# Optimization experiments

Measured on AMD Instinct MI355X. Metric: run time of the kernel, lower is better.

Reference implementation:

```python
import jax, jax.numpy as jnp
import numpy as np

SEGMENT_LENGTHS = [1024, 2048, 4096]
DILATION_RATES = [1, 2, 4]


def setup_inputs() -> dict:
    key = jax.random.key(0)
    kq, kk, kv = jax.random.split(key, 3)
    shape = (2, 4096, 12, 64)  # [batch, seq_len, num_heads, head_dim]
    return {
        "query": jax.random.normal(kq, shape, dtype=jnp.float32),
        "key": jax.random.normal(kk, shape, dtype=jnp.float32),
        "value": jax.random.normal(kv, shape, dtype=jnp.float32),
        "is_causal": 0,
    }


def _group_attention(q, k, v, g, r, offset, is_causal):
    """Dilated segment attention for one head group.

    q/k/v: [b, n, hg, d] (head slice for this group).
    Segments of length g; within each segment attend only at positions
    offset, offset+r, ... (m = g // r tokens). Output scattered back to
    those positions; other positions are zero (LongNet semantics).
    """
    b, n, h, d = q.shape
    s = n // g  # number of segments
    m = g // r  # dilated tokens per segment
    idx = offset + r * jnp.arange(m)
    qs = q.reshape(b, s, g, h, d)[:, :, idx]  # [b, s, m, h, d]
    ks = k.reshape(b, s, g, h, d)[:, :, idx]
    vs = v.reshape(b, s, g, h, d)[:, :, idx]
    scale = 1.0 / jnp.sqrt(jnp.asarray(d, dtype=q.dtype))
    scores = jnp.einsum("bsqhd,bskhd->bshqk", qs, ks) * scale  # [b, s, h, m, m]
    if is_causal:
        mask = jnp.tril(jnp.ones((m, m), dtype=bool))
        scores = jnp.where(mask, scores, jnp.finfo(scores.dtype).min)
    probs = jax.nn.softmax(scores, axis=-1)
    o = jnp.einsum("bshqk,bskhd->bsqhd", probs, vs)  # [b, s, m, h, d]
    out = jnp.zeros((b, s, g, h, d), dtype=q.dtype).at[:, :, idx].set(o)
    return out.reshape(b, n, h, d)


def reference(query, key, value, is_causal):
    # dist not initialized -> sequence-parallel split/gather are identity;
    # forward reduces to ImprovedDilatedAttention on full tensors.
    b, n, h, d = query.shape
    ngroups = len(SEGMENT_LENGTHS)
    hpg = h // ngroups  # heads per group (disjoint head slices)
    causal = bool(is_causal)
    outs = []
    for i, (g, r) in enumerate(zip(SEGMENT_LENGTHS, DILATION_RATES)):
        offset = i % r
        hmin, hmax = i * hpg, (i + 1) * hpg
        outs.append(
            _group_attention(
                query[:, :, hmin:hmax],
                key[:, :, hmin:hmax],
                value[:, :, hmin:hmax],
                g, r, offset, causal,
            )
        )
    return jnp.concatenate(outs, axis=2)  # [b, n, h, d]
```

## Files before the change

### kernel.cpp

```cpp
#include <hip/hip_runtime.h>
#include <hip/hip_bf16.h>

typedef __attribute__((ext_vector_type(8))) short short8;
typedef __attribute__((ext_vector_type(4))) float f32x4;

#define NTILE 16

static __device__ __forceinline__ unsigned pk2(float x, float y) {
  __hip_bfloat162 h = __float22bfloat162_rn(make_float2(x, y));
  unsigned u; __builtin_memcpy(&u, &h, 4); return u;
}

static __device__ __forceinline__ short8 cvt8(float4 a, float4 b) {
  union { unsigned u[4]; short8 s; } r;
  r.u[0] = pk2(a.x, a.y); r.u[1] = pk2(a.z, a.w);
  r.u[2] = pk2(b.x, b.y); r.u[3] = pk2(b.z, b.w);
  return r.s;
}

static __device__ __forceinline__ void gll16(const void* g, void* l) {
  __builtin_amdgcn_global_load_lds(
      (__attribute__((address_space(1))) void*)const_cast<void*>(g),
      (__attribute__((address_space(3))) void*)(l), 16, 0, 0);
}

struct InstInfo { long base0; int stride; };
static __device__ __forceinline__ InstInfo decode_inst(int inst) {
  const int gi    = (inst < 32) ? 0 : ((inst < 48) ? 1 : 2);
  const int local = inst - ((gi == 0) ? 0 : ((gi == 1) ? 32 : 48));
  const int segs  = 4 >> gi;
  const int g     = 1024 << gi;
  const int offs  = gi;
  const int h     = local & 3;
  const int rem   = local >> 2;
  const int seg   = rem & (segs - 1);
  const int b     = rem >> (2 - gi);
  const int hh    = gi * 4 + h;
  InstInfo r;
  r.base0  = ((long)(b * 4096 + seg * g + offs) * 12 + hh) * 64;
  r.stride = (1 << gi) * 768;
  return r;
}

__global__ __launch_bounds__(256)
void pack_kv(const float* __restrict__ Kg, const float* __restrict__ Vg,
             unsigned short* __restrict__ Ks, unsigned short* __restrict__ Vts,
             float* __restrict__ Og)
{
  __shared__ float vtmp[64][65];
  const int tid   = threadIdx.x;
  const int lid   = blockIdx.x;
  const int inst  = lid % 56;
  const int chunk = lid / 56;
  const int gi    = (inst < 32) ? 0 : ((inst < 48) ? 1 : 2);
  InstInfo I = decode_inst(inst);

  {
    const int tok = tid >> 2, part = tid & 3;
    const long ro = I.base0 + (long)(chunk * 64 + tok) * I.stride + part * 16;
    const float4 k0 = *(const float4*)(Kg + ro);
    const float4 k1 = *(const float4*)(Kg + ro + 4);
    const float4 k2 = *(const float4*)(Kg + ro + 8);
    const float4 k3 = *(const float4*)(Kg + ro + 12);
    uint4 ka, kb;
    ka.x = pk2(k0.x,k0.y); ka.y = pk2(k0.z,k0.w); ka.z = pk2(k1.x,k1.y); ka.w = pk2(k1.z,k1.w);
    kb.x = pk2(k2.x,k2.y); kb.y = pk2(k2.z,k2.w); kb.z = pk2(k3.x,k3.y); kb.w = pk2(k3.z,k3.w);
    unsigned short* kd = Ks + ((long)inst*1024 + chunk*64 + tok)*64;
    const int c0 = (2*part)     ^ (tok & 7);
    const int c1 = (2*part + 1) ^ (tok & 7);
    *(uint4*)(kd + c0*8) = ka;
    *(uint4*)(kd + c1*8) = kb;

    const float4 w0 = *(const float4*)(Vg + ro);
    const float4 w1 = *(const float4*)(Vg + ro + 4);
    const float4 w2 = *(const float4*)(Vg + ro + 8);
    const float4 w3 = *(const float4*)(Vg + ro + 12);
    float* c = &vtmp[part*16][0] + tok;
    c[0*65]=w0.x;  c[1*65]=w0.y;  c[2*65]=w0.z;  c[3*65]=w0.w;
    c[4*65]=w1.x;  c[5*65]=w1.y;  c[6*65]=w1.z;  c[7*65]=w1.w;
    c[8*65]=w2.x;  c[9*65]=w2.y;  c[10*65]=w2.z; c[11*65]=w2.w;
    c[12*65]=w3.x; c[13*65]=w3.y; c[14*65]=w3.z; c[15*65]=w3.w;
  }
  __syncthreads();
  {
    const int d = tid >> 2, kp = tid & 3;
    float v[16];
#pragma unroll
    for (int i = 0; i < 16; ++i) v[i] = vtmp[d][kp*16 + i];
    unsigned short* vd = Vts + ((long)inst*64 + d)*1024 + chunk*64;
#pragma unroll
    for (int s = 0; s < 2; ++s) {
      const int pos = (kp*2 + s) ^ (d & 7);
      uint4 w;
      w.x = pk2(v[8*s+0], v[8*s+1]); w.y = pk2(v[8*s+2], v[8*s+3]);
      w.z = pk2(v[8*s+4], v[8*s+5]); w.w = pk2(v[8*s+6], v[8*s+7]);
      *(uint4*)(vd + pos*8) = w;
    }
  }

  const float4 z4 = make_float4(0.f, 0.f, 0.f, 0.f);
  if (gi == 1) {
    for (int i = tid; i < 64*16; i += 256) {
      const int t = i >> 4, pp = i & 15;
      float* op = Og + I.base0 + (long)(chunk*128 + 2*t + 0 - 1) * 768 + pp*4;
      *(float4*)op = z4;
    }
  } else if (gi == 2) {
    for (int i = tid; i < 192*16; i += 256) {
      const int row_i = i >> 4, pp = i & 15;
      const int t = row_i / 3, ddi = row_i - 3*t;
      const int dd = ddi + (ddi >= 2 ? 1 : 0);
      float* op = Og + I.base0 + (long)(chunk*256 + 4*t + dd - 2) * 768 + pp*4;
      *(float4*)op = z4;
    }
  }
}

__global__ __launch_bounds__(256, 2)
void dilated_attn2(const float* __restrict__ Qg,
                   const unsigned short* __restrict__ Ks,
                   const unsigned short* __restrict__ Vts,
                   const int* __restrict__ causal_flag,
                   float* __restrict__ Og)
{
  __shared__ __align__(16) unsigned short K_lds[2][64][64];
  __shared__ __align__(16) unsigned short V_lds[2][64][64];
  __shared__ __align__(16) unsigned short P_lds[4][16][64];

  const int tid  = threadIdx.x;
  const int wave = tid >> 6;
  const int lane = tid & 63;
  const int l15  = lane & 15;
  const int l4   = lane >> 4;
  const int sw   = l15 & 7;

  const int lid  = blockIdx.x;
  const int inst = lid % 56;
  const int qt   = lid / 56;
  InstInfo I = decode_inst(inst);
  const int causal = *causal_flag;

  const float qscale = 0.125f * 1.44269504088896340736f;
  short8 b_q[2][2];
  int qrowf[2];
#pragma unroll
  for (int qf = 0; qf < 2; ++qf) {
    qrowf[qf] = qt*128 + wave*32 + qf*16 + l15;
    const float* qp = Qg + I.base0 + (long)qrowf[qf] * I.stride + l4 * 8;
#pragma unroll
    for (int ks = 0; ks < 2; ++ks) {
      float4 v0 = *(const float4*)(qp + ks*32);
      float4 v1 = *(const float4*)(qp + ks*32 + 4);
      v0.x *= qscale; v0.y *= qscale; v0.z *= qscale; v0.w *= qscale;
      v1.x *= qscale; v1.y *= qscale; v1.z *= qscale; v1.w *= qscale;
      b_q[qf][ks] = cvt8(v0, v1);
    }
  }

  short8 ones8;
  {
    union { unsigned u[4]; short8 s; } r;
    r.u[0] = r.u[1] = r.u[2] = r.u[3] = 0x3F803F80u;
    ones8 = r.s;
  }

  const unsigned short* KsI  = Ks  + (long)inst * (1024*64);
  const unsigned short* VtsI = Vts + (long)inst * (64*1024);
  const int vrow = lane >> 3;
  const int vcol = (lane & 7) * 8;

  const long koffA = (long)(wave*8     + vrow)*64 + vcol;
  const long koffB = (long)((wave+4)*8 + vrow)*64 + vcol;
  const long voffA = (long)(wave*8     + vrow)*1024 + vcol;
  const long voffB = (long)((wave+4)*8 + vrow)*1024 + vcol;
  const int  colA  = ((l4 ^ sw) & 7) * 8;
  const int  colB  = (((4 + l4) ^ sw) & 7) * 8;
  const unsigned short* krow0 = &K_lds[0][l15][0];
  const unsigned short* krow1 = &K_lds[1][l15][0];
  const unsigned short* vrow0 = &V_lds[0][l15][0];
  const unsigned short* vrow1 = &V_lds[1][l15][0];
  unsigned short* pw = &P_lds[wave][l15][0];
  int pwo[4];
#pragma unroll
  for (int n = 0; n < 4; ++n)
    pwo[n] = (((2*n + (l4 >> 1)) ^ sw) & 7)*8 + (l4 & 1)*4;
  const int pro0 = colA;
  const int pro1 = colB;

  f32x4 Oacc[2][4];
  f32x4 accl[2];
#pragma unroll
  for (int qf = 0; qf < 2; ++qf) {
    accl[qf] = (f32x4){0.f,0.f,0.f,0.f};
#pragma unroll
    for (int n = 0; n < 4; ++n) Oacc[qf][n] = (f32x4){0.f,0.f,0.f,0.f};
  }

#define STAGE_G(BUF, KP, VP) do {                                              \
    gll16((KP) + koffA, &K_lds[BUF][wave*8][0]);                               \
    gll16((KP) + koffB, &K_lds[BUF][(wave+4)*8][0]);                           \
    gll16((VP) + voffA, &V_lds[BUF][wave*8][0]);                               \
    gll16((VP) + voffB, &V_lds[BUF][(wave+4)*8][0]);                           \
  } while (0)

#define COMPUTE(CUR, KT) do {                                                  \
    f32x4 S0[4], S1[4];                                                        \
    __builtin_amdgcn_s_setprio(1);                                             \
    _Pragma("unroll")                                                          \
    for (int n = 0; n < 4; ++n) {                                              \
      short8 kA = *(const short8*)(krow##CUR + n*1024 + colA);                 \
      short8 kB = *(const short8*)(krow##CUR + n*1024 + colB);                 \
      f32x4 a0 = (f32x4){0.f,0.f,0.f,0.f};                                     \
      a0 = __builtin_amdgcn_mfma_f32_16x16x32_bf16(kA, b_q[0][0], a0, 0,0,0);  \
      a0 = __builtin_amdgcn_mfma_f32_16x16x32_bf16(kB, b_q[0][1], a0, 0,0,0);  \
      S0[n] = a0;                                                              \
      f32x4 a1 = (f32x4){0.f,0.f,0.f,0.f};                                     \
      a1 = __builtin_amdgcn_mfma_f32_16x16x32_bf16(kA, b_q[1][0], a1, 0,0,0);  \
      a1 = __builtin_amdgcn_mfma_f32_16x16x32_bf16(kB, b_q[1][1], a1, 0,0,0);  \
      S1[n] = a1;                                                              \
    }                                                                          \
    __builtin_amdgcn_s_setprio(0);                                             \
    if (causal) {                                                              \
      _Pragma("unroll")                                                        \
      for (int n = 0; n < 4; ++n)                                              \
        _Pragma("unroll")                                                      \
        for (int j = 0; j < 4; ++j) {                                          \
          int ktok = (KT)*64 + n*16 + l4*4 + j;                                \
          if (ktok > qrowf[0]) S0[n][j] = -INFINITY;                           \
          if (ktok > qrowf[1]) S1[n][j] = -INFINITY;                           \
        }                                                                      \
    }                                                                          \
    short8 ap0a, ap0b, ap1a, ap1b;                                             \
    {                                                                \
      _Pragma("unroll")                                                        \
      for (int n = 0; n < 4; ++n) {                                            \
        unsigned u0 = pk2(__builtin_amdgcn_exp2f(S0[n][0]),                    \
                          __builtin_amdgcn_exp2f(S0[n][1]));                   \
        unsigned u1 = pk2(__builtin_amdgcn_exp2f(S0[n][2]),                    \
                          __builtin_amdgcn_exp2f(S0[n][3]));                   \
        *(uint2*)(pw + pwo[n]) = make_uint2(u0, u1);                           \
      }                                                                        \
      ap0a = *(const short8*)(pw + pro0);                                      \
      ap0b = *(const short8*)(pw + pro1);                                      \
      accl[0] = __builtin_amdgcn_mfma_f32_16x16x32_bf16(ap0a, ones8, accl[0], 0,0,0); \
      accl[0] = __builtin_amdgcn_mfma_f32_16x16x32_bf16(ap0b, ones8, accl[0], 0,0,0); \
    }                                                                          \
    {                                                                \
      _Pragma("unroll")                                                        \
      for (int n = 0; n < 4; ++n) {                                            \
        unsigned u0 = pk2(__builtin_amdgcn_exp2f(S1[n][0]),                    \
                          __builtin_amdgcn_exp2f(S1[n][1]));                   \
        unsigned u1 = pk2(__builtin_amdgcn_exp2f(S1[n][2]),                    \
                          __builtin_amdgcn_exp2f(S1[n][3]));                   \
        *(uint2*)(pw + pwo[n]) = make_uint2(u0, u1);                           \
      }                                                                        \
      ap1a = *(const short8*)(pw + pro0);                                      \
      ap1b = *(const short8*)(pw + pro1);                                      \
      accl[1] = __builtin_amdgcn_mfma_f32_16x16x32_bf16(ap1a, ones8, accl[1], 0,0,0); \
      accl[1] = __builtin_amdgcn_mfma_f32_16x16x32_bf16(ap1b, ones8, accl[1], 0,0,0); \
    }                                                                          \
    _Pragma("unroll")                                                          \
    for (int n = 0; n < 4; ++n) {                                              \
      short8 bv0 = *(const short8*)(vrow##CUR + n*1024 + colA);                \
      short8 bv1 = *(const short8*)(vrow##CUR + n*1024 + colB);                \
      __builtin_amdgcn_s_setprio(1);                                           \
      Oacc[0][n] = __builtin_amdgcn_mfma_f32_16x16x32_bf16(ap0a, bv0, Oacc[0][n], 0,0,0); \
      Oacc[0][n] = __builtin_amdgcn_mfma_f32_16x16x32_bf16(ap0b, bv1, Oacc[0][n], 0,0,0); \
      Oacc[1][n] = __builtin_amdgcn_mfma_f32_16x16x32_bf16(ap1a, bv0, Oacc[1][n], 0,0,0); \
      Oacc[1][n] = __builtin_amdgcn_mfma_f32_16x16x32_bf16(ap1b, bv1, Oacc[1][n], 0,0,0); \
      __builtin_amdgcn_s_setprio(0);                                           \
    }                                                                          \
  } while (0)

  STAGE_G(0, KsI, VtsI);
  __syncthreads();

  const unsigned short* kp1 = KsI + 4096;
  const unsigned short* kp2 = KsI + 8192;
  const unsigned short* vp1 = VtsI + 64;
  const unsigned short* vp2 = VtsI + 128;

  for (int p = 0; p < NTILE/2; ++p) {
    const int kt = 2*p;
    STAGE_G(1, kp1, vp1);
    COMPUTE(0, kt);
    __syncthreads();
    if (p < NTILE/2 - 1) STAGE_G(0, kp2, vp2);
    COMPUTE(1, kt + 1);
    __syncthreads();
    kp1 += 8192; kp2 += 8192; vp1 += 128; vp2 += 128;
  }

  float* ob = Og + I.base0;
#pragma unroll
  for (int qf = 0; qf < 2; ++qf)
#pragma unroll
    for (int j = 0; j < 4; ++j) {
      const float inv = 1.f / accl[qf][j];
      const int qrow = qt*128 + wave*32 + qf*16 + l4*4 + j;
      float* op = ob + (long)qrow * I.stride;
#pragma unroll
      for (int n = 0; n < 4; ++n)
        op[n*16 + l15] = Oacc[qf][n][j] * inv;
    }
}

#define LDP 72
__global__ __launch_bounds__(512, 4)
void dilated_attn_fb(const float* __restrict__ Qg,
                     const float* __restrict__ Kg,
                     const float* __restrict__ Vg,
                     const int* __restrict__ causal_flag,
                     float* __restrict__ Og)
{
  __shared__ __align__(16) unsigned short K_lds[2][64][LDP];
  __shared__ __align__(16) unsigned short Vt_lds[2][64][LDP];
  __shared__ __align__(16) unsigned short P_lds[8][16][LDP];

  const int tid  = threadIdx.x;
  const int wave = tid >> 6;
  const int lane = tid & 63;
  const int l15  = lane & 15;
  const int l4   = lane >> 4;
  const int qt   = blockIdx.x;
  InstInfo I = decode_inst(blockIdx.y);
  const int causal = *causal_flag;

  const float qscale = 0.125f * 1.44269504088896340736f;
  short8 b_q[2];
  {
    const int qrow = qt * 128 + wave * 16 + l15;
    const float* qp = Qg + I.base0 + (long)qrow * I.stride + l4 * 8;
#pragma unroll
    for (int ks = 0; ks < 2; ++ks) {
      float4 v0 = *(const float4*)(qp + ks * 32);
      float4 v1 = *(const float4*)(qp + ks * 32 + 4);
      v0.x *= qscale; v0.y *= qscale; v0.z *= qscale; v0.w *= qscale;
      v1.x *= qscale; v1.y *= qscale; v1.z *= qscale; v1.w *= qscale;
      b_q[ks] = cvt8(v0, v1);
    }
  }
  float m_run = -INFINITY, l_run = 0.f;
  f32x4 Oacc[4];
#pragma unroll
  for (int n = 0; n < 4; ++n) Oacc[n] = (f32x4){0.f,0.f,0.f,0.f};
  const int tt  = tid >> 3;
  const int cb8 = tid & 7;
  const float* kbase = Kg + I.base0 + cb8 * 8;
  const float* vbase = Vg + I.base0 + cb8 * 8;
#define STAGE_FB(BUF, A0, A1, W0, W1) do {                                     \
    *(short8*)&K_lds[BUF][tt][cb8 * 8] = cvt8(A0, A1);                         \
    unsigned p01 = pk2(W0.x, W0.y), p23 = pk2(W0.z, W0.w);                     \
    unsigned p45 = pk2(W1.x, W1.y), p67 = pk2(W1.z, W1.w);                     \
    const int col = (((tt >> 3) ^ cb8) << 3) | (tt & 7);                       \
    Vt_lds[BUF][cb8*8+0][col] = (unsigned short)(p01 & 0xffff);                \
    Vt_lds[BUF][cb8*8+1][col] = (unsigned short)(p01 >> 16);                   \
    Vt_lds[BUF][cb8*8+2][col] = (unsigned short)(p23 & 0xffff);                \
    Vt_lds[BUF][cb8*8+3][col] = (unsigned short)(p23 >> 16);                   \
    Vt_lds[BUF][cb8*8+4][col] = (unsigned short)(p45 & 0xffff);                \
    Vt_lds[BUF][cb8*8+5][col] = (unsigned short)(p45 >> 16);                   \
    Vt_lds[BUF][cb8*8+6][col] = (unsigned short)(p67 & 0xffff);                \
    Vt_lds[BUF][cb8*8+7][col] = (unsigned short)(p67 >> 16);                   \
  } while (0)
  {
    const long ro = (long)tt * I.stride;
    float4 k0 = *(const float4*)(kbase + ro);
    float4 k1 = *(const float4*)(kbase + ro + 4);
    float4 w0 = *(const float4*)(vbase + ro);
    float4 w1 = *(const float4*)(vbase + ro + 4);
    STAGE_FB(0, k0, k1, w0, w1);
  }
  __syncthreads();
  const int qrow_me = qt * 128 + wave * 16 + l15;
  for (int kt = 0; kt < NTILE; ++kt) {
    const int bsel = kt & 1;
    float4 nk0, nk1, nw0, nw1;
    const bool have_next = (kt + 1 < NTILE);
    if (have_next) {
      const long ro = (long)((kt + 1) * 64 + tt) * I.stride;
      nk0 = *(const float4*)(kbase + ro);
      nk1 = *(const float4*)(kbase + ro + 4);
      nw0 = *(const float4*)(vbase + ro);
      nw1 = *(const float4*)(vbase + ro + 4);
    }
    f32x4 S[4];
#pragma unroll
    for (int n = 0; n < 4; ++n) {
      short8 ak0 = *(const short8*)&K_lds[bsel][n*16 + l15][l4*8];
      short8 ak1 = *(const short8*)&K_lds[bsel][n*16 + l15][32 + l4*8];
      f32x4 acc = (f32x4){0.f,0.f,0.f,0.f};
      acc = __builtin_amdgcn_mfma_f32_16x16x32_bf16(ak0, b_q[0], acc, 0,0,0);
      acc = __builtin_amdgcn_mfma_f32_16x16x32_bf16(ak1, b_q[1], acc, 0,0,0);
      S[n] = acc;
    }
    if (causal) {
#pragma unroll
      for (int n = 0; n < 4; ++n)
#pragma unroll
        for (int j = 0; j < 4; ++j) {
          int ktok = kt*64 + n*16 + l4*4 + j;
          if (ktok > qrow_me) S[n][j] = -INFINITY;
        }
    }
    float pmax = S[0][0];
#pragma unroll
    for (int n = 0; n < 4; ++n)
#pragma unroll
      for (int j = 0; j < 4; ++j) pmax = fmaxf(pmax, S[n][j]);
    pmax = fmaxf(pmax, __shfl_xor(pmax, 16));
    pmax = fmaxf(pmax, __shfl_xor(pmax, 32));
    if (!__all(pmax - m_run <= 8.f)) {
      float mn = fmaxf(m_run, pmax);
      float corr = exp2f(m_run - mn);
      m_run = mn; l_run *= corr;
      float cq[4];
#pragma unroll
      for (int j = 0; j < 4; ++j) cq[j] = __shfl(corr, l4*4 + j, 16);
#pragma unroll
      for (int n = 0; n < 4; ++n)
#pragma unroll
        for (int j = 0; j < 4; ++j) Oacc[n][j] *= cq[j];
    }
    float psum = 0.f; unsigned up[4][2];
#pragma unroll
    for (int n = 0; n < 4; ++n)
#pragma unroll
      for (int s = 0; s < 2; ++s) {
        float p0 = exp2f(S[n][2*s]   - m_run);
        float p1 = exp2f(S[n][2*s+1] - m_run);
        psum += p0 + p1; up[n][s] = pk2(p0, p1);
      }
    l_run += psum;
#pragma unroll
    for (int n = 0; n < 4; ++n)
      *(uint2*)&P_lds[wave][l15][n*16 + l4*4] = make_uint2(up[n][0], up[n][1]);
    {
      short8 ap0 = *(const short8*)&P_lds[wave][l15][l4*8];
      short8 ap1 = *(const short8*)&P_lds[wave][l15][32 + l4*8];
#pragma unroll
      for (int n = 0; n < 4; ++n) {
        const int dsw = (2*n + (l15 >> 3)) & 7;
        short8 bv0 = *(const short8*)&Vt_lds[bsel][n*16 + l15][((l4 ^ dsw) & 7)*8];
        short8 bv1 = *(const short8*)&Vt_lds[bsel][n*16 + l15][(((4 + l4) ^ dsw) & 7)*8];
        Oacc[n] = __builtin_amdgcn_mfma_f32_16x16x32_bf16(ap0, bv0, Oacc[n], 0,0,0);
        Oacc[n] = __builtin_amdgcn_mfma_f32_16x16x32_bf16(ap1, bv1, Oacc[n], 0,0,0);
      }
    }
    if (have_next) STAGE_FB(bsel ^ 1, nk0, nk1, nw0, nw1);
    __syncthreads();
  }
  l_run += __shfl_xor(l_run, 16);
  l_run += __shfl_xor(l_run, 32);
  float lq[4];
#pragma unroll
  for (int j = 0; j < 4; ++j) lq[j] = __shfl(l_run, l4*4 + j, 16);
  float* ob = Og + I.base0;
#pragma unroll
  for (int j = 0; j < 4; ++j) {
    const float inv = 1.f / lq[j];
    const int qrow = qt*128 + wave*16 + l4*4 + j;
    float* op = ob + (long)qrow * I.stride;
#pragma unroll
    for (int n = 0; n < 4; ++n)
      op[n*16 + l15] = Oacc[n][j] * inv;
  }
}

extern "C" void kernel_launch(void* const* d_in, const int* in_sizes, int n_in,
                              void* d_out, int out_size, void* d_ws, size_t ws_size,
                              hipStream_t stream) {
  const float* Q = (const float*)d_in[0];
  const float* K = (const float*)d_in[1];
  const float* V = (const float*)d_in[2];
  const int* causal = (const int*)d_in[3];
  float* out = (float*)d_out;

  const size_t per = 56ull * 1024 * 64;
  const size_t need_pack = 2 * per * sizeof(unsigned short);

  if (ws_size >= need_pack) {
    unsigned short* Ks  = (unsigned short*)d_ws;
    unsigned short* Vts = Ks + per;
    pack_kv<<<896, 256, 0, stream>>>(K, V, Ks, Vts, out);
    dilated_attn2<<<448, 256, 0, stream>>>(Q, Ks, Vts, causal, out);
  } else {
    (void)hipMemsetAsync(d_out, 0, (size_t)out_size * sizeof(float), stream);
    dilated_attn_fb<<<dim3(8, 56), 512, 0, stream>>>(Q, K, V, causal, out);
  }
}
```

Before: 40.22 us.

## Split each KV tile across two wave groups and merge partial outputs in LDS

Doubles the block to 512 threads. Each of the two 4-wave halves processes a different 32-key half of every 64-key tile for the same 128 queries, which halves each wave's MFMA and exp work per tile. The partial O accumulators and row sums from the second half are reduced through LDS in the epilogue. The no-max softmax makes the split-K merge a plain sum. In exchange it adds an extra barrier, LDS traffic in the epilogue, and higher register and LDS pressure per CU.

```diff
diff --git a/kernel.cpp b/kernel.cpp
--- a/kernel.cpp
+++ b/kernel.cpp
@@ -116,16 +116,16 @@
   }
 }
 
-__global__ __launch_bounds__(256, 2)
+__global__ __launch_bounds__(512, 2)
 void dilated_attn2(const float* __restrict__ Qg,
                    const unsigned short* __restrict__ Ks,
                    const unsigned short* __restrict__ Vts,
                    const int* __restrict__ causal_flag,
                    float* __restrict__ Og)
 {
-  __shared__ __align__(16) unsigned short K_lds[2][64][64];
-  __shared__ __align__(16) unsigned short V_lds[2][64][64];
-  __shared__ __align__(16) unsigned short P_lds[4][16][64];
+  __shared__ __align__(16) unsigned short KV_lds[4][64][64];
+  __shared__ __align__(16) unsigned short P_lds[8][16][64];
+  __shared__ float Lx[4][32];
 
   const int tid  = threadIdx.x;
   const int wave = tid >> 6;
@@ -133,6 +133,9 @@
   const int l15  = lane & 15;
   const int l4   = lane >> 4;
   const int sw   = l15 & 7;
+  const int qh   = wave & 3;
+  const int kh   = wave >> 2;
+  const int khb  = kh * 32;
 
   const int lid  = blockIdx.x;
   const int inst = lid % 56;
@@ -145,7 +148,7 @@
   int qrowf[2];
 #pragma unroll
   for (int qf = 0; qf < 2; ++qf) {
-    qrowf[qf] = qt*128 + wave*32 + qf*16 + l15;
+    qrowf[qf] = qt*128 + qh*32 + qf*16 + l15;
     const float* qp = Qg + I.base0 + (long)qrowf[qf] * I.stride + l4 * 8;
 #pragma unroll
     for (int ks = 0; ks < 2; ++ks) {
@@ -169,23 +172,21 @@
   const int vrow = lane >> 3;
   const int vcol = (lane & 7) * 8;
 
-  const long koffA = (long)(wave*8     + vrow)*64 + vcol;
-  const long koffB = (long)((wave+4)*8 + vrow)*64 + vcol;
-  const long voffA = (long)(wave*8     + vrow)*1024 + vcol;
-  const long voffB = (long)((wave+4)*8 + vrow)*1024 + vcol;
-  const int  colA  = ((l4 ^ sw) & 7) * 8;
-  const int  colB  = (((4 + l4) ^ sw) & 7) * 8;
-  const unsigned short* krow0 = &K_lds[0][l15][0];
-  const unsigned short* krow1 = &K_lds[1][l15][0];
-  const unsigned short* vrow0 = &V_lds[0][l15][0];
-  const unsigned short* vrow1 = &V_lds[1][l15][0];
+  const long koff = (long)(wave*8 + vrow)*64 + vcol;
+  const long voff = (long)(wave*8 + vrow)*1024 + vcol;
+  const int  colA = ((l4 ^ sw) & 7) * 8;
+  const int  colB = (((4 + l4) ^ sw) & 7) * 8;
+  const int  vcb  = (((kh*4 + l4) ^ sw) & 7) * 8;
+  const unsigned short* krow0 = &KV_lds[0][khb + l15][0];
+  const unsigned short* krow1 = &KV_lds[1][khb + l15][0];
+  const unsigned short* vb0   = &KV_lds[2][l15][0];
+  const unsigned short* vb1   = &KV_lds[3][l15][0];
   unsigned short* pw = &P_lds[wave][l15][0];
-  int pwo[4];
-#pragma unroll
-  for (int n = 0; n < 4; ++n)
+  int pwo[2];
+#pragma unroll
+  for (int n = 0; n < 2; ++n)
     pwo[n] = (((2*n + (l4 >> 1)) ^ sw) & 7)*8 + (l4 & 1)*4;
-  const int pro0 = colA;
-  const int pro1 = colB;
+  const int pro = colA;
 
   f32x4 Oacc[2][4];
   f32x4 accl[2];
@@ -197,19 +198,17 @@
   }
 
 #define STAGE_G(BUF, KP, VP) do {                                              \
-    gll16((KP) + koffA, &K_lds[BUF][wave*8][0]);                               \
-    gll16((KP) + koffB, &K_lds[BUF][(wave+4)*8][0]);                           \
-    gll16((VP) + voffA, &V_lds[BUF][wave*8][0]);                               \
-    gll16((VP) + voffB, &V_lds[BUF][(wave+4)*8][0]);                           \
+    gll16((KP) + koff, &KV_lds[BUF][wave*8][0]);                               \
+    gll16((VP) + voff, &KV_lds[2+(BUF)][wave*8][0]);                           \
   } while (0)
 
 #define COMPUTE(CUR, KT) do {                                                  \
-    f32x4 S0[4], S1[4];                                                        \
+    f32x4 S0[2], S1[2];                                                        \
     __builtin_amdgcn_s_setprio(1);                                             \
     _Pragma("unroll")                                                          \
-    for (int n = 0; n < 4; ++n) {                                              \
-      short8 kA = *(const short8*)(krow##CUR + n*1024 + colA);                 \
-      short8 kB = *(const short8*)(krow##CUR + n*1024 + colB);                 \
+    for (int n = 0; n < 2; ++n) {                                              \
+      short8 kA = *(const short8*)(krow##CUR + n*16*64 + colA);                \
+      short8 kB = *(const short8*)(krow##CUR + n*16*64 + colB);                \
       f32x4 a0 = (f32x4){0.f,0.f,0.f,0.f};                                     \
       a0 = __builtin_amdgcn_mfma_f32_16x16x32_bf16(kA, b_q[0][0], a0, 0,0,0);  \
       a0 = __builtin_amdgcn_mfma_f32_16x16x32_bf16(kB, b_q[0][1], a0, 0,0,0);  \
@@ -222,52 +221,45 @@
     __builtin_amdgcn_s_setprio(0);                                             \
     if (causal) {                                                              \
       _Pragma("unroll")                                                        \
-      for (int n = 0; n < 4; ++n)                                              \
+      for (int n = 0; n < 2; ++n)                                              \
         _Pragma("unroll")                                                      \
         for (int j = 0; j < 4; ++j) {                                          \
-          int ktok = (KT)*64 + n*16 + l4*4 + j;                                \
+          int ktok = (KT)*64 + khb + n*16 + l4*4 + j;                          \
           if (ktok > qrowf[0]) S0[n][j] = -INFINITY;                           \
           if (ktok > qrowf[1]) S1[n][j] = -INFINITY;                           \
         }                                                                      \
     }                                                                          \
-    short8 ap0a, ap0b, ap1a, ap1b;                                             \
+    short8 ap0, ap1;                                                           \
     {                                                                \
       _Pragma("unroll")                                                        \
-      for (int n = 0; n < 4; ++n) {                                            \
+      for (int n = 0; n < 2; ++n) {                                            \
         unsigned u0 = pk2(__builtin_amdgcn_exp2f(S0[n][0]),                    \
                           __builtin_amdgcn_exp2f(S0[n][1]));                   \
         unsigned u1 = pk2(__builtin_amdgcn_exp2f(S0[n][2]),                    \
                           __builtin_amdgcn_exp2f(S0[n][3]));                   \
         *(uint2*)(pw + pwo[n]) = make_uint2(u0, u1);                           \
       }                                                                        \
-      ap0a = *(const short8*)(pw + pro0);                                      \
-      ap0b = *(const short8*)(pw + pro1);                                      \
-      accl[0] = __builtin_amdgcn_mfma_f32_16x16x32_bf16(ap0a, ones8, accl[0], 0,0,0); \
-      accl[0] = __builtin_amdgcn_mfma_f32_16x16x32_bf16(ap0b, ones8, accl[0], 0,0,0); \
+      ap0 = *(const short8*)(pw + pro);                                        \
+      accl[0] = __builtin_amdgcn_mfma_f32_16x16x32_bf16(ap0, ones8, accl[0], 0,0,0); \
     }                                                                          \
     {                                                                \
       _Pragma("unroll")                                                        \
-      for (int n = 0; n < 4; ++n) {                                            \
+      for (int n = 0; n < 2; ++n) {                                            \
         unsigned u0 = pk2(__builtin_amdgcn_exp2f(S1[n][0]),                    \
                           __builtin_amdgcn_exp2f(S1[n][1]));                   \
         unsigned u1 = pk2(__builtin_amdgcn_exp2f(S1[n][2]),                    \
                           __builtin_amdgcn_exp2f(S1[n][3]));                   \
         *(uint2*)(pw + pwo[n]) = make_uint2(u0, u1);                           \
       }                                                                        \
-      ap1a = *(const short8*)(pw + pro0);                                      \
-      ap1b = *(const short8*)(pw + pro1);                                      \
-      accl[1] = __builtin_amdgcn_mfma_f32_16x16x32_bf16(ap1a, ones8, accl[1], 0,0,0); \
-      accl[1] = __builtin_amdgcn_mfma_f32_16x16x32_bf16(ap1b, ones8, accl[1], 0,0,0); \
+      ap1 = *(const short8*)(pw + pro);                                        \
+      accl[1] = __builtin_amdgcn_mfma_f32_16x16x32_bf16(ap1, ones8, accl[1], 0,0,0); \
     }                                                                          \
     _Pragma("unroll")                                                          \
     for (int n = 0; n < 4; ++n) {                                              \
-      short8 bv0 = *(const short8*)(vrow##CUR + n*1024 + colA);                \
-      short8 bv1 = *(const short8*)(vrow##CUR + n*1024 + colB);                \
+      short8 bv = *(const short8*)(vb##CUR + n*16*64 + vcb);                   \
       __builtin_amdgcn_s_setprio(1);                                           \
-      Oacc[0][n] = __builtin_amdgcn_mfma_f32_16x16x32_bf16(ap0a, bv0, Oacc[0][n], 0,0,0); \
-      Oacc[0][n] = __builtin_amdgcn_mfma_f32_16x16x32_bf16(ap0b, bv1, Oacc[0][n], 0,0,0); \
-      Oacc[1][n] = __builtin_amdgcn_mfma_f32_16x16x32_bf16(ap1a, bv0, Oacc[1][n], 0,0,0); \
-      Oacc[1][n] = __builtin_amdgcn_mfma_f32_16x16x32_bf16(ap1b, bv1, Oacc[1][n], 0,0,0); \
+      Oacc[0][n] = __builtin_amdgcn_mfma_f32_16x16x32_bf16(ap0, bv, Oacc[0][n], 0,0,0); \
+      Oacc[1][n] = __builtin_amdgcn_mfma_f32_16x16x32_bf16(ap1, bv, Oacc[1][n], 0,0,0); \
       __builtin_amdgcn_s_setprio(0);                                           \
     }                                                                          \
   } while (0)
@@ -291,18 +283,36 @@
     kp1 += 8192; kp2 += 8192; vp1 += 128; vp2 += 128;
   }
 
-  float* ob = Og + I.base0;
-#pragma unroll
-  for (int qf = 0; qf < 2; ++qf)
-#pragma unroll
-    for (int j = 0; j < 4; ++j) {
-      const float inv = 1.f / accl[qf][j];
-      const int qrow = qt*128 + wave*32 + qf*16 + l4*4 + j;
-      float* op = ob + (long)qrow * I.stride;
-#pragma unroll
-      for (int n = 0; n < 4; ++n)
-        op[n*16 + l15] = Oacc[qf][n][j] * inv;
-    }
+  float* Ox = (float*)&KV_lds[0][0][0];
+  if (kh == 1) {
+#pragma unroll
+    for (int qf = 0; qf < 2; ++qf)
+#pragma unroll
+      for (int j = 0; j < 4; ++j) {
+        const int r = qf*16 + l4*4 + j;
+        float* dst = Ox + (qh*32 + r)*64;
+#pragma unroll
+        for (int n = 0; n < 4; ++n) dst[n*16 + l15] = Oacc[qf][n][j];
+        if (l15 == 0) Lx[qh][r] = accl[qf][j];
+      }
+  }
+  __syncthreads();
+  if (kh == 0) {
+    float* ob = Og + I.base0;
+#pragma unroll
+    for (int qf = 0; qf < 2; ++qf)
+#pragma unroll
+      for (int j = 0; j < 4; ++j) {
+        const int r = qf*16 + l4*4 + j;
+        const float* src = Ox + (qh*32 + r)*64;
+        const float inv = 1.f / (accl[qf][j] + Lx[qh][r]);
+        const int qrow = qt*128 + qh*32 + r;
+        float* op = ob + (long)qrow * I.stride;
+#pragma unroll
+        for (int n = 0; n < 4; ++n)
+          op[n*16 + l15] = (Oacc[qf][n][j] + src[n*16 + l15]) * inv;
+      }
+  }
 }
 
 #define LDP 72
@@ -482,7 +492,7 @@
     unsigned short* Ks  = (unsigned short*)d_ws;
     unsigned short* Vts = Ks + per;
     pack_kv<<<896, 256, 0, stream>>>(K, V, Ks, Vts, out);
-    dilated_attn2<<<448, 256, 0, stream>>>(Q, Ks, Vts, causal, out);
+    dilated_attn2<<<448, 512, 0, stream>>>(Q, Ks, Vts, causal, out);
   } else {
     (void)hipMemsetAsync(d_out, 0, (size_t)out_size * sizeof(float), stream);
     dilated_attn_fb<<<dim3(8, 56), 512, 0, stream>>>(Q, K, V, causal, out);
```

Result: slower. 41.15 us (+2.3%).

## Load K/V fragments directly from global into registers, drop LDS staging

Applied to the files above, without the earlier changes.

The attention kernel no longer stages K and V tiles into shared memory with global_load_lds and barriers. Each lane now loads its MFMA operand fragments straight from global memory into registers, double-buffered across tiles. The pre-pass drops its XOR swizzle and writes K and transposed V in a plain layout. This removes LDS traffic and the per-tile __syncthreads, at the cost of more register pressure and repeated global/L2 reads, since the four waves each fetch the same K/V data.

```diff
diff --git a/kernel.cpp b/kernel.cpp
--- a/kernel.cpp
+++ b/kernel.cpp
@@ -16,12 +16,6 @@
   r.u[0] = pk2(a.x, a.y); r.u[1] = pk2(a.z, a.w);
   r.u[2] = pk2(b.x, b.y); r.u[3] = pk2(b.z, b.w);
   return r.s;
-}
-
-static __device__ __forceinline__ void gll16(const void* g, void* l) {
-  __builtin_amdgcn_global_load_lds(
-      (__attribute__((address_space(1))) void*)const_cast<void*>(g),
-      (__attribute__((address_space(3))) void*)(l), 16, 0, 0);
 }
 
 struct InstInfo { long base0; int stride; };
@@ -65,11 +59,8 @@
     uint4 ka, kb;
     ka.x = pk2(k0.x,k0.y); ka.y = pk2(k0.z,k0.w); ka.z = pk2(k1.x,k1.y); ka.w = pk2(k1.z,k1.w);
     kb.x = pk2(k2.x,k2.y); kb.y = pk2(k2.z,k2.w); kb.z = pk2(k3.x,k3.y); kb.w = pk2(k3.z,k3.w);
-    unsigned short* kd = Ks + ((long)inst*1024 + chunk*64 + tok)*64;
-    const int c0 = (2*part)     ^ (tok & 7);
-    const int c1 = (2*part + 1) ^ (tok & 7);
-    *(uint4*)(kd + c0*8) = ka;
-    *(uint4*)(kd + c1*8) = kb;
+    unsigned short* kd = Ks + ((long)inst*1024 + chunk*64 + tok)*64 + part*16;
+    *(uint4*)kd = ka; *(uint4*)(kd + 8) = kb;
 
     const float4 w0 = *(const float4*)(Vg + ro);
     const float4 w1 = *(const float4*)(Vg + ro + 4);
@@ -87,15 +78,13 @@
     float v[16];
 #pragma unroll
     for (int i = 0; i < 16; ++i) v[i] = vtmp[d][kp*16 + i];
-    unsigned short* vd = Vts + ((long)inst*64 + d)*1024 + chunk*64;
-#pragma unroll
-    for (int s = 0; s < 2; ++s) {
-      const int pos = (kp*2 + s) ^ (d & 7);
-      uint4 w;
-      w.x = pk2(v[8*s+0], v[8*s+1]); w.y = pk2(v[8*s+2], v[8*s+3]);
-      w.z = pk2(v[8*s+4], v[8*s+5]); w.w = pk2(v[8*s+6], v[8*s+7]);
-      *(uint4*)(vd + pos*8) = w;
-    }
+    unsigned short* vd = Vts + ((long)inst*64 + d)*1024 + chunk*64 + kp*16;
+    uint4 wa, wb;
+    wa.x = pk2(v[0], v[1]);  wa.y = pk2(v[2], v[3]);
+    wa.z = pk2(v[4], v[5]);  wa.w = pk2(v[6], v[7]);
+    wb.x = pk2(v[8], v[9]);  wb.y = pk2(v[10], v[11]);
+    wb.z = pk2(v[12], v[13]); wb.w = pk2(v[14], v[15]);
+    *(uint4*)vd = wa; *(uint4*)(vd + 8) = wb;
   }
 
   const float4 z4 = make_float4(0.f, 0.f, 0.f, 0.f);
@@ -123,8 +112,6 @@
                    const int* __restrict__ causal_flag,
                    float* __restrict__ Og)
 {
-  __shared__ __align__(16) unsigned short K_lds[2][64][64];
-  __shared__ __align__(16) unsigned short V_lds[2][64][64];
   __shared__ __align__(16) unsigned short P_lds[4][16][64];
 
   const int tid  = threadIdx.x;
@@ -164,28 +151,16 @@
     ones8 = r.s;
   }
 
-  const unsigned short* KsI  = Ks  + (long)inst * (1024*64);
-  const unsigned short* VtsI = Vts + (long)inst * (64*1024);
-  const int vrow = lane >> 3;
-  const int vcol = (lane & 7) * 8;
-
-  const long koffA = (long)(wave*8     + vrow)*64 + vcol;
-  const long koffB = (long)((wave+4)*8 + vrow)*64 + vcol;
-  const long voffA = (long)(wave*8     + vrow)*1024 + vcol;
-  const long voffB = (long)((wave+4)*8 + vrow)*1024 + vcol;
-  const int  colA  = ((l4 ^ sw) & 7) * 8;
-  const int  colB  = (((4 + l4) ^ sw) & 7) * 8;
-  const unsigned short* krow0 = &K_lds[0][l15][0];
-  const unsigned short* krow1 = &K_lds[1][l15][0];
-  const unsigned short* vrow0 = &V_lds[0][l15][0];
-  const unsigned short* vrow1 = &V_lds[1][l15][0];
+  const unsigned short* KsI  = Ks  + (long)inst * (1024*64) + l15*64 + l4*8;
+  const unsigned short* VtsI = Vts + (long)inst * (64*1024) + (long)l15*1024 + l4*8;
+
   unsigned short* pw = &P_lds[wave][l15][0];
   int pwo[4];
 #pragma unroll
   for (int n = 0; n < 4; ++n)
     pwo[n] = (((2*n + (l4 >> 1)) ^ sw) & 7)*8 + (l4 & 1)*4;
-  const int pro0 = colA;
-  const int pro1 = colB;
+  const int pro0 = ((l4 ^ sw) & 7) * 8;
+  const int pro1 = (((4 + l4) ^ sw) & 7) * 8;
 
   f32x4 Oacc[2][4];
   f32x4 accl[2];
@@ -196,27 +171,33 @@
     for (int n = 0; n < 4; ++n) Oacc[qf][n] = (f32x4){0.f,0.f,0.f,0.f};
   }
 
-#define STAGE_G(BUF, KP, VP) do {                                              \
-    gll16((KP) + koffA, &K_lds[BUF][wave*8][0]);                               \
-    gll16((KP) + koffB, &K_lds[BUF][(wave+4)*8][0]);                           \
-    gll16((VP) + voffA, &V_lds[BUF][wave*8][0]);                               \
-    gll16((VP) + voffB, &V_lds[BUF][(wave+4)*8][0]);                           \
+  short8 kA_A[4], kB_A[4], vA_A[4], vB_A[4];
+  short8 kA_B[4], kB_B[4], vA_B[4], vB_B[4];
+
+#define LOADT(SUF, KT) do {                                                    \
+    const unsigned short* kb = KsI  + (long)(KT) * 4096;                       \
+    const unsigned short* vb = VtsI + (long)(KT) * 64;                         \
+    _Pragma("unroll")                                                          \
+    for (int n = 0; n < 4; ++n) {                                              \
+      kA_##SUF[n] = *(const short8*)(kb + n*1024);                             \
+      kB_##SUF[n] = *(const short8*)(kb + n*1024 + 32);                        \
+      vA_##SUF[n] = *(const short8*)(vb + (long)n*16384);                      \
+      vB_##SUF[n] = *(const short8*)(vb + (long)n*16384 + 32);                 \
+    }                                                                          \
   } while (0)
 
-#define COMPUTE(CUR, KT) do {                                                  \
+#define COMPUTE(SUF, KT) do {                                                  \
     f32x4 S0[4], S1[4];                                                        \
     __builtin_amdgcn_s_setprio(1);                                             \
     _Pragma("unroll")                                                          \
     for (int n = 0; n < 4; ++n) {                                              \
-      short8 kA = *(const short8*)(krow##CUR + n*1024 + colA);                 \
-      short8 kB = *(const short8*)(krow##CUR + n*1024 + colB);                 \
       f32x4 a0 = (f32x4){0.f,0.f,0.f,0.f};                                     \
-      a0 = __builtin_amdgcn_mfma_f32_16x16x32_bf16(kA, b_q[0][0], a0, 0,0,0);  \
-      a0 = __builtin_amdgcn_mfma_f32_16x16x32_bf16(kB, b_q[0][1], a0, 0,0,0);  \
+      a0 = __builtin_amdgcn_mfma_f32_16x16x32_bf16(kA_##SUF[n], b_q[0][0], a0, 0,0,0); \
+      a0 = __builtin_amdgcn_mfma_f32_16x16x32_bf16(kB_##SUF[n], b_q[0][1], a0, 0,0,0); \
       S0[n] = a0;                                                              \
       f32x4 a1 = (f32x4){0.f,0.f,0.f,0.f};                                     \
-      a1 = __builtin_amdgcn_mfma_f32_16x16x32_bf16(kA, b_q[1][0], a1, 0,0,0);  \
-      a1 = __builtin_amdgcn_mfma_f32_16x16x32_bf16(kB, b_q[1][1], a1, 0,0,0);  \
+      a1 = __builtin_amdgcn_mfma_f32_16x16x32_bf16(kA_##SUF[n], b_q[1][0], a1, 0,0,0); \
+      a1 = __builtin_amdgcn_mfma_f32_16x16x32_bf16(kB_##SUF[n], b_q[1][1], a1, 0,0,0); \
       S1[n] = a1;                                                              \
     }                                                                          \
     __builtin_amdgcn_s_setprio(0);                                             \
@@ -231,7 +212,7 @@
         }                                                                      \
     }                                                                          \
     short8 ap0a, ap0b, ap1a, ap1b;                                             \
-    {                                                                \
+    {                                                                          \
       _Pragma("unroll")                                                        \
       for (int n = 0; n < 4; ++n) {                                            \
         unsigned u0 = pk2(__builtin_amdgcn_exp2f(S0[n][0]),                    \
@@ -245,7 +226,7 @@
       accl[0] = __builtin_amdgcn_mfma_f32_16x16x32_bf16(ap0a, ones8, accl[0], 0,0,0); \
       accl[0] = __builtin_amdgcn_mfma_f32_16x16x32_bf16(ap0b, ones8, accl[0], 0,0,0); \
     }                                                                          \
-    {                                                                \
+    {                                                                          \
       _Pragma("unroll")                                                        \
       for (int n = 0; n < 4; ++n) {                                            \
         unsigned u0 = pk2(__builtin_amdgcn_exp2f(S1[n][0]),                    \
@@ -261,34 +242,22 @@
     }                                                                          \
     _Pragma("unroll")                                                          \
     for (int n = 0; n < 4; ++n) {                                              \
-      short8 bv0 = *(const short8*)(vrow##CUR + n*1024 + colA);                \
-      short8 bv1 = *(const short8*)(vrow##CUR + n*1024 + colB);                \
       __builtin_amdgcn_s_setprio(1);                                           \
-      Oacc[0][n] = __builtin_amdgcn_mfma_f32_16x16x32_bf16(ap0a, bv0, Oacc[0][n], 0,0,0); \
-      Oacc[0][n] = __builtin_amdgcn_mfma_f32_16x16x32_bf16(ap0b, bv1, Oacc[0][n], 0,0,0); \
-      Oacc[1][n] = __builtin_amdgcn_mfma_f32_16x16x32_bf16(ap1a, bv0, Oacc[1][n], 0,0,0); \
-      Oacc[1][n] = __builtin_amdgcn_mfma_f32_16x16x32_bf16(ap1b, bv1, Oacc[1][n], 0,0,0); \
+      Oacc[0][n] = __builtin_amdgcn_mfma_f32_16x16x32_bf16(ap0a, vA_##SUF[n], Oacc[0][n], 0,0,0); \
+      Oacc[0][n] = __builtin_amdgcn_mfma_f32_16x16x32_bf16(ap0b, vB_##SUF[n], Oacc[0][n], 0,0,0); \
+      Oacc[1][n] = __builtin_amdgcn_mfma_f32_16x16x32_bf16(ap1a, vA_##SUF[n], Oacc[1][n], 0,0,0); \
+      Oacc[1][n] = __builtin_amdgcn_mfma_f32_16x16x32_bf16(ap1b, vB_##SUF[n], Oacc[1][n], 0,0,0); \
       __builtin_amdgcn_s_setprio(0);                                           \
     }                                                                          \
   } while (0)
 
-  STAGE_G(0, KsI, VtsI);
-  __syncthreads();
-
-  const unsigned short* kp1 = KsI + 4096;
-  const unsigned short* kp2 = KsI + 8192;
-  const unsigned short* vp1 = VtsI + 64;
-  const unsigned short* vp2 = VtsI + 128;
-
+  LOADT(A, 0);
   for (int p = 0; p < NTILE/2; ++p) {
     const int kt = 2*p;
-    STAGE_G(1, kp1, vp1);
-    COMPUTE(0, kt);
-    __syncthreads();
-    if (p < NTILE/2 - 1) STAGE_G(0, kp2, vp2);
-    COMPUTE(1, kt + 1);
-    __syncthreads();
-    kp1 += 8192; kp2 += 8192; vp1 += 128; vp2 += 128;
+    LOADT(B, kt + 1);
+    COMPUTE(A, kt);
+    if (p < NTILE/2 - 1) LOADT(A, kt + 2);
+    COMPUTE(B, kt + 1);
   }
 
   float* ob = Og + I.base0;
```

New measurement: 76.11 us. +89.3%, slower.

## Switch attention kernel to 32x32x16 MFMA with register-only P transposition

Applied to the files above, without the earlier changes.

Rewrites the main attention kernel to use 32x32x16 bf16 MFMA tiles instead of 16x16x32. Each lane now owns one query row, so the probability matrix is reshaped into the PV operand layout with permlane32_swap rather than a round trip through shared memory. The row sum is accumulated in VALU and combined across lane halves with a shuffle, replacing the ones-vector MFMA. The aim is to drop the P LDS traffic and extra MFMAs, at the cost of more register pressure from 16-wide accumulators.

```diff
diff --git a/kernel.cpp b/kernel.cpp
--- a/kernel.cpp
+++ b/kernel.cpp
@@ -3,6 +3,8 @@
 
 typedef __attribute__((ext_vector_type(8))) short short8;
 typedef __attribute__((ext_vector_type(4))) float f32x4;
+typedef __attribute__((ext_vector_type(16))) float f32x16;
+typedef __attribute__((ext_vector_type(2))) unsigned uint2v;
 
 #define NTILE 16
 
@@ -125,14 +127,13 @@
 {
   __shared__ __align__(16) unsigned short K_lds[2][64][64];
   __shared__ __align__(16) unsigned short V_lds[2][64][64];
-  __shared__ __align__(16) unsigned short P_lds[4][16][64];
 
   const int tid  = threadIdx.x;
   const int wave = tid >> 6;
   const int lane = tid & 63;
-  const int l15  = lane & 15;
-  const int l4   = lane >> 4;
-  const int sw   = l15 & 7;
+  const int l31  = lane & 31;
+  const int h    = lane >> 5;
+  const int swk  = l31 & 7;
 
   const int lid  = blockIdx.x;
   const int inst = lid % 56;
@@ -140,61 +141,42 @@
   InstInfo I = decode_inst(inst);
   const int causal = *causal_flag;
 
+  const int q = qt*128 + wave*32 + l31;
+
   const float qscale = 0.125f * 1.44269504088896340736f;
-  short8 b_q[2][2];
-  int qrowf[2];
-#pragma unroll
-  for (int qf = 0; qf < 2; ++qf) {
-    qrowf[qf] = qt*128 + wave*32 + qf*16 + l15;
-    const float* qp = Qg + I.base0 + (long)qrowf[qf] * I.stride + l4 * 8;
-#pragma unroll
-    for (int ks = 0; ks < 2; ++ks) {
-      float4 v0 = *(const float4*)(qp + ks*32);
-      float4 v1 = *(const float4*)(qp + ks*32 + 4);
+  short8 b_q[4];
+  {
+    const float* qp = Qg + I.base0 + (long)q * I.stride + h*8;
+#pragma unroll
+    for (int ds = 0; ds < 4; ++ds) {
+      float4 v0 = *(const float4*)(qp + ds*16);
+      float4 v1 = *(const float4*)(qp + ds*16 + 4);
       v0.x *= qscale; v0.y *= qscale; v0.z *= qscale; v0.w *= qscale;
       v1.x *= qscale; v1.y *= qscale; v1.z *= qscale; v1.w *= qscale;
-      b_q[qf][ks] = cvt8(v0, v1);
-    }
-  }
-
-  short8 ones8;
-  {
-    union { unsigned u[4]; short8 s; } r;
-    r.u[0] = r.u[1] = r.u[2] = r.u[3] = 0x3F803F80u;
-    ones8 = r.s;
-  }
-
-  const unsigned short* KsI  = Ks  + (long)inst * (1024*64);
-  const unsigned short* VtsI = Vts + (long)inst * (64*1024);
+      b_q[ds] = cvt8(v0, v1);
+    }
+  }
+
+  int offs[4];
+#pragma unroll
+  for (int i = 0; i < 4; ++i) offs[i] = (((i*2 + h) ^ swk) & 7) * 8;
+
+  const unsigned short* KsSt  = Ks  + (long)inst * (1024*64);
+  const unsigned short* VtSt  = Vts + (long)inst * (64*1024);
   const int vrow = lane >> 3;
   const int vcol = (lane & 7) * 8;
-
   const long koffA = (long)(wave*8     + vrow)*64 + vcol;
   const long koffB = (long)((wave+4)*8 + vrow)*64 + vcol;
   const long voffA = (long)(wave*8     + vrow)*1024 + vcol;
   const long voffB = (long)((wave+4)*8 + vrow)*1024 + vcol;
-  const int  colA  = ((l4 ^ sw) & 7) * 8;
-  const int  colB  = (((4 + l4) ^ sw) & 7) * 8;
-  const unsigned short* krow0 = &K_lds[0][l15][0];
-  const unsigned short* krow1 = &K_lds[1][l15][0];
-  const unsigned short* vrow0 = &V_lds[0][l15][0];
-  const unsigned short* vrow1 = &V_lds[1][l15][0];
-  unsigned short* pw = &P_lds[wave][l15][0];
-  int pwo[4];
-#pragma unroll
-  for (int n = 0; n < 4; ++n)
-    pwo[n] = (((2*n + (l4 >> 1)) ^ sw) & 7)*8 + (l4 & 1)*4;
-  const int pro0 = colA;
-  const int pro1 = colB;
-
-  f32x4 Oacc[2][4];
-  f32x4 accl[2];
-#pragma unroll
-  for (int qf = 0; qf < 2; ++qf) {
-    accl[qf] = (f32x4){0.f,0.f,0.f,0.f};
-#pragma unroll
-    for (int n = 0; n < 4; ++n) Oacc[qf][n] = (f32x4){0.f,0.f,0.f,0.f};
-  }
+
+  const unsigned short* kb0 = &K_lds[0][l31][0];
+  const unsigned short* kb1 = &K_lds[1][l31][0];
+  const unsigned short* vb0 = &V_lds[0][l31][0];
+  const unsigned short* vb1 = &V_lds[1][l31][0];
+
+  f32x16 O0 = {}, O1 = {};
+  float psum = 0.f;
 
 #define STAGE_G(BUF, KP, VP) do {                                              \
     gll16((KP) + koffA, &K_lds[BUF][wave*8][0]);                               \
@@ -203,82 +185,89 @@
     gll16((VP) + voffB, &V_lds[BUF][(wave+4)*8][0]);                           \
   } while (0)
 
+#define PACK8(S, U) do {                                                       \
+    _Pragma("unroll")                                                          \
+    for (int g = 0; g < 4; ++g) {                                              \
+      float e0 = __builtin_amdgcn_exp2f(S[4*g+0]);                             \
+      float e1 = __builtin_amdgcn_exp2f(S[4*g+1]);                             \
+      float e2 = __builtin_amdgcn_exp2f(S[4*g+2]);                             \
+      float e3 = __builtin_amdgcn_exp2f(S[4*g+3]);                             \
+      psum += (e0 + e1) + (e2 + e3);                                           \
+      U[2*g]   = pk2(e0, e1);                                                  \
+      U[2*g+1] = pk2(e2, e3);                                                  \
+    }                                                                          \
+  } while (0)
+
+#define MKFRAG(DST, Ua, Ub, Uc, Ud) do {                                       \
+    uint2v r02 = __builtin_amdgcn_permlane32_swap((Ua), (Uc), false, false);   \
+    uint2v r13 = __builtin_amdgcn_permlane32_swap((Ub), (Ud), false, false);   \
+    union { unsigned w[4]; short8 s; } f_;                                     \
+    f_.w[0] = r02[0]; f_.w[1] = r13[0]; f_.w[2] = r02[1]; f_.w[3] = r13[1];    \
+    DST = f_.s;                                                                \
+  } while (0)
+
 #define COMPUTE(CUR, KT) do {                                                  \
-    f32x4 S0[4], S1[4];                                                        \
+    f32x16 S0 = {}, S1 = {};                                                   \
     __builtin_amdgcn_s_setprio(1);                                             \
     _Pragma("unroll")                                                          \
-    for (int n = 0; n < 4; ++n) {                                              \
-      short8 kA = *(const short8*)(krow##CUR + n*1024 + colA);                 \
-      short8 kB = *(const short8*)(krow##CUR + n*1024 + colB);                 \
-      f32x4 a0 = (f32x4){0.f,0.f,0.f,0.f};                                     \
-      a0 = __builtin_amdgcn_mfma_f32_16x16x32_bf16(kA, b_q[0][0], a0, 0,0,0);  \
-      a0 = __builtin_amdgcn_mfma_f32_16x16x32_bf16(kB, b_q[0][1], a0, 0,0,0);  \
-      S0[n] = a0;                                                              \
-      f32x4 a1 = (f32x4){0.f,0.f,0.f,0.f};                                     \
-      a1 = __builtin_amdgcn_mfma_f32_16x16x32_bf16(kA, b_q[1][0], a1, 0,0,0);  \
-      a1 = __builtin_amdgcn_mfma_f32_16x16x32_bf16(kB, b_q[1][1], a1, 0,0,0);  \
-      S1[n] = a1;                                                              \
+    for (int ds = 0; ds < 4; ++ds) {                                           \
+      short8 k0 = *(const short8*)(kb##CUR + offs[ds]);                        \
+      short8 k1 = *(const short8*)(kb##CUR + 2048 + offs[ds]);                 \
+      S0 = __builtin_amdgcn_mfma_f32_32x32x16_bf16(k0, b_q[ds], S0, 0,0,0);    \
+      S1 = __builtin_amdgcn_mfma_f32_32x32x16_bf16(k1, b_q[ds], S1, 0,0,0);    \
     }                                                                          \
     __builtin_amdgcn_s_setprio(0);                                             \
     if (causal) {                                                              \
       _Pragma("unroll")                                                        \
-      for (int n = 0; n < 4; ++n)                                              \
-        _Pragma("unroll")                                                      \
-        for (int j = 0; j < 4; ++j) {                                          \
-          int ktok = (KT)*64 + n*16 + l4*4 + j;                                \
-          if (ktok > qrowf[0]) S0[n][j] = -INFINITY;                           \
-          if (ktok > qrowf[1]) S1[n][j] = -INFINITY;                           \
-        }                                                                      \
-    }                                                                          \
-    short8 ap0a, ap0b, ap1a, ap1b;                                             \
-    {                                                                \
-      _Pragma("unroll")                                                        \
-      for (int n = 0; n < 4; ++n) {                                            \
-        unsigned u0 = pk2(__builtin_amdgcn_exp2f(S0[n][0]),                    \
-                          __builtin_amdgcn_exp2f(S0[n][1]));                   \
-        unsigned u1 = pk2(__builtin_amdgcn_exp2f(S0[n][2]),                    \
-                          __builtin_amdgcn_exp2f(S0[n][3]));                   \
-        *(uint2*)(pw + pwo[n]) = make_uint2(u0, u1);                           \
+      for (int j = 0; j < 16; ++j) {                                           \
+        int kt0 = (KT)*64 + (j&3) + 8*(j>>2) + 4*h;                            \
+        if (kt0      > q) S0[j] = -INFINITY;                                   \
+        if (kt0 + 32 > q) S1[j] = -INFINITY;                                   \
       }                                                                        \
-      ap0a = *(const short8*)(pw + pro0);                                      \
-      ap0b = *(const short8*)(pw + pro1);                                      \
-      accl[0] = __builtin_amdgcn_mfma_f32_16x16x32_bf16(ap0a, ones8, accl[0], 0,0,0); \
-      accl[0] = __builtin_amdgcn_mfma_f32_16x16x32_bf16(ap0b, ones8, accl[0], 0,0,0); \
-    }                                                                          \
-    {                                                                \
-      _Pragma("unroll")                                                        \
-      for (int n = 0; n < 4; ++n) {                                            \
-        unsigned u0 = pk2(__builtin_amdgcn_exp2f(S1[n][0]),                    \
-                          __builtin_amdgcn_exp2f(S1[n][1]));                   \
-        unsigned u1 = pk2(__builtin_amdgcn_exp2f(S1[n][2]),                    \
-                          __builtin_amdgcn_exp2f(S1[n][3]));                   \
-        *(uint2*)(pw + pwo[n]) = make_uint2(u0, u1);                           \
-      }                                                                        \
-      ap1a = *(const short8*)(pw + pro0);                                      \
-      ap1b = *(const short8*)(pw + pro1);                                      \
-      accl[1] = __builtin_amdgcn_mfma_f32_16x16x32_bf16(ap1a, ones8, accl[1], 0,0,0); \
-      accl[1] = __builtin_amdgcn_mfma_f32_16x16x32_bf16(ap1b, ones8, accl[1], 0,0,0); \
-    }                                                                          \
-    _Pragma("unroll")                                                          \
-    for (int n = 0; n < 4; ++n) {                                              \
-      short8 bv0 = *(const short8*)(vrow##CUR + n*1024 + colA);                \
-      short8 bv1 = *(const short8*)(vrow##CUR + n*1024 + colB);                \
-      __builtin_amdgcn_s_setprio(1);                                           \
-      Oacc[0][n] = __builtin_amdgcn_mfma_f32_16x16x32_bf16(ap0a, bv0, Oacc[0][n], 0,0,0); \
-      Oacc[0][n] = __builtin_amdgcn_mfma_f32_16x16x32_bf16(ap0b, bv1, Oacc[0][n], 0,0,0); \
-      Oacc[1][n] = __builtin_amdgcn_mfma_f32_16x16x32_bf16(ap1a, bv0, Oacc[1][n], 0,0,0); \
-      Oacc[1][n] = __builtin_amdgcn_mfma_f32_16x16x32_bf16(ap1b, bv1, Oacc[1][n], 0,0,0); \
-      __builtin_amdgcn_s_setprio(0);                                           \
-    }                                                                          \
+    }                                                                          \
+    unsigned u0[8], u1[8];                                                     \
+    PACK8(S0, u0);                                                             \
+    PACK8(S1, u1);                                                             \
+    short8 P0, P1, P2, P3;                                                     \
+    MKFRAG(P0, u0[0], u0[1], u0[2], u0[3]);                                    \
+    MKFRAG(P1, u0[4], u0[5], u0[6], u0[7]);                                    \
+    MKFRAG(P2, u1[0], u1[1], u1[2], u1[3]);                                    \
+    MKFRAG(P3, u1[4], u1[5], u1[6], u1[7]);                                    \
+    __builtin_amdgcn_s_setprio(1);                                             \
+    {                                                                          \
+      short8 v0 = *(const short8*)(vb##CUR + offs[0]);                         \
+      short8 v1 = *(const short8*)(vb##CUR + 2048 + offs[0]);                  \
+      O0 = __builtin_amdgcn_mfma_f32_32x32x16_bf16(v0, P0, O0, 0,0,0);         \
+      O1 = __builtin_amdgcn_mfma_f32_32x32x16_bf16(v1, P0, O1, 0,0,0);         \
+    }                                                                          \
+    {                                                                          \
+      short8 v0 = *(const short8*)(vb##CUR + offs[1]);                         \
+      short8 v1 = *(const short8*)(vb##CUR + 2048 + offs[1]);                  \
+      O0 = __builtin_amdgcn_mfma_f32_32x32x16_bf16(v0, P1, O0, 0,0,0);         \
+      O1 = __builtin_amdgcn_mfma_f32_32x32x16_bf16(v1, P1, O1, 0,0,0);         \
+    }                                                                          \
+    {                                                                          \
+      short8 v0 = *(const short8*)(vb##CUR + offs[2]);                         \
+      short8 v1 = *(const short8*)(vb##CUR + 2048 + offs[2]);                  \
+      O0 = __builtin_amdgcn_mfma_f32_32x32x16_bf16(v0, P2, O0, 0,0,0);         \
+      O1 = __builtin_amdgcn_mfma_f32_32x32x16_bf16(v1, P2, O1, 0,0,0);         \
+    }                                                                          \
+    {                                                                          \
+      short8 v0 = *(const short8*)(vb##CUR + offs[3]);                         \
+      short8 v1 = *(const short8*)(vb##CUR + 2048 + offs[3]);                  \
+      O0 = __builtin_amdgcn_mfma_f32_32x32x16_bf16(v0, P3, O0, 0,0,0);         \
+      O1 = __builtin_amdgcn_mfma_f32_32x32x16_bf16(v1, P3, O1, 0,0,0);         \
+    }                                                                          \
+    __builtin_amdgcn_s_setprio(0);                                             \
   } while (0)
 
-  STAGE_G(0, KsI, VtsI);
+  STAGE_G(0, KsSt, VtSt);
   __syncthreads();
 
-  const unsigned short* kp1 = KsI + 4096;
-  const unsigned short* kp2 = KsI + 8192;
-  const unsigned short* vp1 = VtsI + 64;
-  const unsigned short* vp2 = VtsI + 128;
+  const unsigned short* kp1 = KsSt + 4096;
+  const unsigned short* kp2 = KsSt + 8192;
+  const unsigned short* vp1 = VtSt + 64;
+  const unsigned short* vp2 = VtSt + 128;
 
   for (int p = 0; p < NTILE/2; ++p) {
     const int kt = 2*p;
@@ -291,18 +280,17 @@
     kp1 += 8192; kp2 += 8192; vp1 += 128; vp2 += 128;
   }
 
-  float* ob = Og + I.base0;
-#pragma unroll
-  for (int qf = 0; qf < 2; ++qf)
-#pragma unroll
-    for (int j = 0; j < 4; ++j) {
-      const float inv = 1.f / accl[qf][j];
-      const int qrow = qt*128 + wave*32 + qf*16 + l4*4 + j;
-      float* op = ob + (long)qrow * I.stride;
-#pragma unroll
-      for (int n = 0; n < 4; ++n)
-        op[n*16 + l15] = Oacc[qf][n][j] * inv;
-    }
+  const float l = psum + __shfl_xor(psum, 32);
+  const float inv = 1.f / l;
+  float* op = Og + I.base0 + (long)q * I.stride;
+#pragma unroll
+  for (int g = 0; g < 4; ++g) {
+    const int d0 = 8*g + 4*h;
+    float4 w0 = make_float4(O0[4*g]*inv, O0[4*g+1]*inv, O0[4*g+2]*inv, O0[4*g+3]*inv);
+    float4 w1 = make_float4(O1[4*g]*inv, O1[4*g+1]*inv, O1[4*g+2]*inv, O1[4*g+3]*inv);
+    *(float4*)(op + d0)      = w0;
+    *(float4*)(op + 32 + d0) = w1;
+  }
 }
 
 #define LDP 72
```

After: 41.55 us. 3.3% more time.
